# Kernel optimization log

Hardware: AMD Instinct MI355X
Metric: run time of the kernel (lower is better)

## Reference

```python
import jax, jax.numpy as jnp
import numpy as np

B, S, D = 2, 2048, 1024
H, DH = 16, 64
FF = 4 * D
EPS = 1e-5
SCALE = 1.0 / np.sqrt(DH)


def setup_inputs() -> dict:
    key = jax.random.key(0)
    ks = jax.random.split(key, 8)
    std = 0.02
    return {
        "x": jax.random.normal(ks[0], (B, S, D), jnp.float32),
        "ln1_g": jnp.ones((D,), jnp.float32),
        "ln1_b": jnp.zeros((D,), jnp.float32),
        "w_qkv": jax.random.normal(ks[1], (D, 3 * H * DH), jnp.float32) * std,
        "b_qkv": jnp.zeros((3 * H * DH,), jnp.float32),
        "w_ao": jax.random.normal(ks[2], (H * DH, D), jnp.float32) * std,
        "b_ao": jnp.zeros((D,), jnp.float32),
        "ln2_g": jnp.ones((D,), jnp.float32),
        "ln2_b": jnp.zeros((D,), jnp.float32),
        "w_fc": jax.random.normal(ks[3], (D, FF), jnp.float32) * std,
        "b_fc": jnp.zeros((FF,), jnp.float32),
        "w_proj": jax.random.normal(ks[4], (FF, D), jnp.float32) * std,
        "b_proj": jnp.zeros((D,), jnp.float32),
    }


def _layernorm(x, g, b):
    mu = jnp.mean(x, axis=-1, keepdims=True)
    var = jnp.mean(jnp.square(x - mu), axis=-1, keepdims=True)
    return (x - mu) * jax.lax.rsqrt(var + EPS) * g + b


def reference(x, ln1_g, ln1_b, w_qkv, b_qkv, w_ao, b_ao,
              ln2_g, ln2_b, w_fc, b_fc, w_proj, b_proj):
    # pre-LN attention
    h = _layernorm(x, ln1_g, ln1_b)
    qkv = h @ w_qkv + b_qkv                      # [B,S,3*H*DH]
    q, k, v = jnp.split(qkv, 3, axis=-1)
    def heads(t):                                 # [B,S,H*DH] -> [B,H,S,DH]
        return t.reshape(B, S, H, DH).transpose(0, 2, 1, 3)
    q, k, v = heads(q), heads(k), heads(v)
    scores = jnp.einsum("bhsd,bhtd->bhst", q, k) * SCALE  # full [B,H,S,S]
    probs = jax.nn.softmax(scores, axis=-1)
    attn = jnp.einsum("bhst,bhtd->bhsd", probs, v)        # [B,H,S,DH]
    attn = attn.transpose(0, 2, 1, 3).reshape(B, S, H * DH)
    attn = attn @ w_ao + b_ao
    x = x + attn
    # pre-LN MLP (exact erf GELU, matches nn.GELU())
    h = _layernorm(x, ln2_g, ln2_b)
    h = jax.nn.gelu(h @ w_fc + b_fc, approximate=False)
    h = h @ w_proj + b_proj
    return x + h
```

## Files before the change

### kernel.cpp

```cpp
#include <hip/hip_runtime.h>
#include <hip/hip_bf16.h>

using short8 = __attribute__((ext_vector_type(8))) short;
using f32x4  = __attribute__((ext_vector_type(4))) float;

#define DEV __device__ __forceinline__

DEV unsigned short f2b(float f) {
  union { float f; unsigned u; } cv; cv.f = f;
  unsigned r = (cv.u + 0x7fffu + ((cv.u >> 16) & 1u)) >> 16;
  return (unsigned short)r;
}

typedef const __attribute__((address_space(1))) unsigned int* gp1;
typedef __attribute__((address_space(3))) unsigned int* lp3;
DEV void gl16(const void* g, void* l) {
  __builtin_amdgcn_global_load_lds((gp1)g, (lp3)l, 16, 0, 0);
}

__global__ void k_tcvt(const float* __restrict__ src, unsigned short* __restrict__ dst,
                       int K, int N) {
  __shared__ float tile[32][33];
  int n0 = blockIdx.x * 32, k0 = blockIdx.y * 32;
  int tx = threadIdx.x, ty = threadIdx.y;
#pragma unroll
  for (int j = 0; j < 4; ++j)
    tile[ty + j * 8][tx] = src[(size_t)(k0 + ty + j * 8) * N + (n0 + tx)];
  __syncthreads();
#pragma unroll
  for (int j = 0; j < 4; ++j)
    dst[(size_t)(n0 + ty + j * 8) * K + (k0 + tx)] = f2b(tile[tx][ty + j * 8]);
}

__global__ void k_tv(const unsigned short* __restrict__ src, unsigned short* __restrict__ dst) {
  __shared__ unsigned short tile[32][33];
  int d0 = blockIdx.x * 32, s0 = blockIdx.y * 32;
  size_t base = (size_t)blockIdx.z * 2048 * 64;
  int tx = threadIdx.x, ty = threadIdx.y;
#pragma unroll
  for (int j = 0; j < 4; ++j)
    tile[ty + j * 8][tx] = src[base + (size_t)(s0 + ty + j * 8) * 64 + (d0 + tx)];
  __syncthreads();
#pragma unroll
  for (int j = 0; j < 4; ++j)
    dst[base + (size_t)(d0 + ty + j * 8) * 2048 + (s0 + tx)] = tile[tx][ty + j * 8];
}

__global__ __launch_bounds__(256) void k_ln(const float* __restrict__ x,
                                            const float* __restrict__ g,
                                            const float* __restrict__ b,
                                            unsigned short* __restrict__ y) {
  int row = blockIdx.x, tid = threadIdx.x;
  float4 v = reinterpret_cast<const float4*>(x + (size_t)row * 1024)[tid];
  float s  = v.x + v.y + v.z + v.w;
  float s2 = v.x * v.x + v.y * v.y + v.z * v.z + v.w * v.w;
#pragma unroll
  for (int m = 1; m < 64; m <<= 1) { s += __shfl_xor(s, m); s2 += __shfl_xor(s2, m); }
  __shared__ float ps[8];
  int w = tid >> 6;
  if ((tid & 63) == 0) { ps[w] = s; ps[4 + w] = s2; }
  __syncthreads();
  s  = ps[0] + ps[1] + ps[2] + ps[3];
  s2 = ps[4] + ps[5] + ps[6] + ps[7];
  float mu   = s * (1.0f / 1024.0f);
  float var  = fmaxf(s2 * (1.0f / 1024.0f) - mu * mu, 0.f);
  float rstd = rsqrtf(var + 1e-5f);
  float4 gv = reinterpret_cast<const float4*>(g)[tid];
  float4 bv = reinterpret_cast<const float4*>(b)[tid];
  ushort4 o;
  o.x = f2b((v.x - mu) * rstd * gv.x + bv.x);
  o.y = f2b((v.y - mu) * rstd * gv.y + bv.y);
  o.z = f2b((v.z - mu) * rstd * gv.z + bv.z);
  o.w = f2b((v.w - mu) * rstd * gv.w + bv.w);
  reinterpret_cast<ushort4*>(y + (size_t)row * 1024)[tid] = o;
}

enum { EPI_QKV = 0, EPI_RESID = 1, EPI_GELU = 2 };

template <int EPI>
__global__ __launch_bounds__(512, 2) void k_gemm256(
    const unsigned short* __restrict__ A, const unsigned short* __restrict__ BT,
    const float* __restrict__ bias, int M, int N, int K,
    unsigned short* __restrict__ outb,
    unsigned short* __restrict__ qb, unsigned short* __restrict__ kb,
    unsigned short* __restrict__ vb) {
  __shared__ __align__(16) unsigned short Abuf[2][256][64];
  __shared__ __align__(16) unsigned short Bbuf[2][256][64];
  int nx = gridDim.x, nwg = nx * gridDim.y;
  int w0 = blockIdx.y * nx + blockIdx.x;
  int id = (w0 & 7) * (nwg >> 3) + (w0 >> 3);
  int bx = id % nx, by = id / nx;
  int m0 = by * 256, n0 = bx * 256;
  int tid = threadIdx.x;
  int lane = tid & 63, wid = tid >> 6;
  int wm = wid >> 2, wn = wid & 3;
  int l15 = lane & 15, g = lane >> 4;
  int swl = l15 & 7;
  int lrow = lane >> 3;
  int lchunk = (lane & 7) ^ lrow;
  const unsigned short* Asrc = A  + (size_t)(m0 + wid * 32 + lrow) * K + lchunk * 8;
  const unsigned short* Bsrc = BT + (size_t)(n0 + wid * 32 + lrow) * K + lchunk * 8;
  auto stage = [&](int buf, int k0) {
#pragma unroll
    for (int i = 0; i < 4; ++i)
      gl16(Asrc + k0 + (size_t)i * 8 * K, &Abuf[buf][wid * 32 + i * 8][0]);
#pragma unroll
    for (int i = 0; i < 4; ++i)
      gl16(Bsrc + k0 + (size_t)i * 8 * K, &Bbuf[buf][wid * 32 + i * 8][0]);
  };
  f32x4 acc[8][4] = {};
  int nt = K >> 6;
  stage(0, 0);
  stage(1, 64);
  asm volatile("s_waitcnt vmcnt(8)" ::: "memory");
  __builtin_amdgcn_sched_barrier(0);
  __builtin_amdgcn_s_barrier();
  int cur = 0;
  for (int t = 0; t < nt; ++t) {
    const unsigned short (*As)[64] = Abuf[cur];
    const unsigned short (*Bs)[64] = Bbuf[cur];
    short8 a0[8], b0[4], a1[8], b1[4];
#pragma unroll
    for (int mi = 0; mi < 8; ++mi)
      a0[mi] = *reinterpret_cast<const short8*>(&As[wm * 128 + mi * 16 + l15][(g ^ swl) * 8]);
#pragma unroll
    for (int ni = 0; ni < 4; ++ni)
      b0[ni] = *reinterpret_cast<const short8*>(&Bs[wn * 64 + ni * 16 + l15][(g ^ swl) * 8]);
    __builtin_amdgcn_s_setprio(1);
#pragma unroll
    for (int mi = 0; mi < 8; ++mi)
#pragma unroll
      for (int ni = 0; ni < 4; ++ni)
        acc[mi][ni] = __builtin_amdgcn_mfma_f32_16x16x32_bf16(a0[mi], b0[ni], acc[mi][ni], 0, 0, 0);
    __builtin_amdgcn_s_setprio(0);
#pragma unroll
    for (int mi = 0; mi < 8; ++mi)
      a1[mi] = *reinterpret_cast<const short8*>(&As[wm * 128 + mi * 16 + l15][((4 + g) ^ swl) * 8]);
#pragma unroll
    for (int ni = 0; ni < 4; ++ni)
      b1[ni] = *reinterpret_cast<const short8*>(&Bs[wn * 64 + ni * 16 + l15][((4 + g) ^ swl) * 8]);
    asm volatile("s_waitcnt lgkmcnt(0)" ::: "memory");
    __builtin_amdgcn_sched_barrier(0);
    __builtin_amdgcn_s_barrier();
    __builtin_amdgcn_sched_barrier(0);
    if (t + 2 < nt) stage(cur, (t + 2) << 6);
    __builtin_amdgcn_s_setprio(1);
#pragma unroll
    for (int mi = 0; mi < 8; ++mi)
#pragma unroll
      for (int ni = 0; ni < 4; ++ni)
        acc[mi][ni] = __builtin_amdgcn_mfma_f32_16x16x32_bf16(a1[mi], b1[ni], acc[mi][ni], 0, 0, 0);
    __builtin_amdgcn_s_setprio(0);
    if (t + 2 < nt) {
      asm volatile("s_waitcnt vmcnt(8)" ::: "memory");
    } else if (t + 1 < nt) {
      asm volatile("s_waitcnt vmcnt(0)" ::: "memory");
    }
    __builtin_amdgcn_sched_barrier(0);
    __builtin_amdgcn_s_barrier();
    cur ^= 1;
  }
#pragma unroll
  for (int mi = 0; mi < 8; ++mi) {
#pragma unroll
    for (int ni = 0; ni < 4; ++ni) {
      int row0 = m0 + wm * 128 + mi * 16 + g * 4;
      int col  = n0 + wn * 64 + ni * 16 + l15;
      float bcol = bias[col];
#pragma unroll
      for (int j = 0; j < 4; ++j) {
        int r = row0 + j;
        float vv = acc[mi][ni][j] + bcol;
        if (EPI == EPI_QKV) {
          int which = col >> 10;
          int hc = col & 1023;
          int h = hc >> 6, d = hc & 63;
          int bb = r >> 11, ss = r & 2047;
          size_t idx = (((size_t)(bb * 16 + h)) * 2048 + ss) * 64 + d;
          unsigned short bv_ = f2b(which == 0 ? vv * 0.18033688011112042f : vv);
          if (which == 0)      qb[idx] = bv_;
          else if (which == 1) kb[idx] = bv_;
          else                 vb[idx] = bv_;
        } else {
          float ge = 0.5f * vv * (1.0f + erff(vv * 0.70710678118654752f));
          outb[(size_t)r * N + col] = f2b(ge);
        }
      }
    }
  }
}

__global__ __launch_bounds__(512) void k_gemm512(
    const unsigned short* __restrict__ A, const unsigned short* __restrict__ BT,
    const float* __restrict__ bias, int M, int N, int K,
    float* __restrict__ outf, const float* __restrict__ resid) {
  __shared__ __align__(16) unsigned short Abuf[2][128][64];
  __shared__ __align__(16) unsigned short Bbuf[2][128][64];
  int nx = gridDim.x, nwg = nx * gridDim.y;
  int w0 = blockIdx.y * nx + blockIdx.x;
  int id = (w0 & 7) * (nwg >> 3) + (w0 >> 3);
  int bx = id % nx, by = id / nx;
  int m0 = by * 128, n0 = bx * 128;
  int tid = threadIdx.x;
  int lane = tid & 63, wid = tid >> 6;
  int wm = wid >> 2, wn = wid & 3;
  int l15 = lane & 15, g = lane >> 4;
  int swl = l15 & 7;
  int lrow = lane >> 3;
  int lchunk = (lane & 7) ^ lrow;
  const unsigned short* Asrc = A  + (size_t)(m0 + wid * 16 + lrow) * K + lchunk * 8;
  const unsigned short* Bsrc = BT + (size_t)(n0 + wid * 16 + lrow) * K + lchunk * 8;
  auto stage = [&](int buf, int k0) {
#pragma unroll
    for (int i = 0; i < 2; ++i)
      gl16(Asrc + k0 + (size_t)i * 8 * K, &Abuf[buf][wid * 16 + i * 8][0]);
#pragma unroll
    for (int i = 0; i < 2; ++i)
      gl16(Bsrc + k0 + (size_t)i * 8 * K, &Bbuf[buf][wid * 16 + i * 8][0]);
  };
  f32x4 acc[4][2] = {};
  int nt = K >> 6;
  stage(0, 0);
  stage(1, 64);
  asm volatile("s_waitcnt vmcnt(4)" ::: "memory");
  __builtin_amdgcn_sched_barrier(0);
  __builtin_amdgcn_s_barrier();
  int cur = 0;
  for (int t = 0; t < nt; ++t) {
    const unsigned short (*As)[64] = Abuf[cur];
    const unsigned short (*Bs)[64] = Bbuf[cur];
    short8 a0[4], b0[2], a1[4], b1[2];
#pragma unroll
    for (int mi = 0; mi < 4; ++mi)
      a0[mi] = *reinterpret_cast<const short8*>(&As[wm * 64 + mi * 16 + l15][(g ^ swl) * 8]);
#pragma unroll
    for (int ni = 0; ni < 2; ++ni)
      b0[ni] = *reinterpret_cast<const short8*>(&Bs[wn * 32 + ni * 16 + l15][(g ^ swl) * 8]);
    __builtin_amdgcn_s_setprio(1);
#pragma unroll
    for (int mi = 0; mi < 4; ++mi)
#pragma unroll
      for (int ni = 0; ni < 2; ++ni)
        acc[mi][ni] = __builtin_amdgcn_mfma_f32_16x16x32_bf16(a0[mi], b0[ni], acc[mi][ni], 0, 0, 0);
    __builtin_amdgcn_s_setprio(0);
#pragma unroll
    for (int mi = 0; mi < 4; ++mi)
      a1[mi] = *reinterpret_cast<const short8*>(&As[wm * 64 + mi * 16 + l15][((4 + g) ^ swl) * 8]);
#pragma unroll
    for (int ni = 0; ni < 2; ++ni)
      b1[ni] = *reinterpret_cast<const short8*>(&Bs[wn * 32 + ni * 16 + l15][((4 + g) ^ swl) * 8]);
    asm volatile("s_waitcnt lgkmcnt(0)" ::: "memory");
    __builtin_amdgcn_sched_barrier(0);
    __builtin_amdgcn_s_barrier();
    __builtin_amdgcn_sched_barrier(0);
    if (t + 2 < nt) stage(cur, (t + 2) << 6);
    __builtin_amdgcn_s_setprio(1);
#pragma unroll
    for (int mi = 0; mi < 4; ++mi)
#pragma unroll
      for (int ni = 0; ni < 2; ++ni)
        acc[mi][ni] = __builtin_amdgcn_mfma_f32_16x16x32_bf16(a1[mi], b1[ni], acc[mi][ni], 0, 0, 0);
    __builtin_amdgcn_s_setprio(0);
    if (t + 2 < nt) {
      asm volatile("s_waitcnt vmcnt(4)" ::: "memory");
    } else if (t + 1 < nt) {
      asm volatile("s_waitcnt vmcnt(0)" ::: "memory");
    }
    __builtin_amdgcn_sched_barrier(0);
    __builtin_amdgcn_s_barrier();
    cur ^= 1;
  }
#pragma unroll
  for (int mi = 0; mi < 4; ++mi) {
#pragma unroll
    for (int ni = 0; ni < 2; ++ni) {
      int row0 = m0 + wm * 64 + mi * 16 + g * 4;
      int col  = n0 + wn * 32 + ni * 16 + l15;
      float bcol = bias[col];
#pragma unroll
      for (int j = 0; j < 4; ++j) {
        size_t idx = (size_t)(row0 + j) * N + col;
        outf[idx] = acc[mi][ni][j] + bcol + resid[idx];
      }
    }
  }
}

__global__ __launch_bounds__(256) void k_attn(
    const unsigned short* __restrict__ qb, const unsigned short* __restrict__ kb,
    const unsigned short* __restrict__ vt, unsigned short* __restrict__ attn_out) {
  __shared__ __align__(16) unsigned short Ks[64][64];
  __shared__ __align__(16) unsigned short Vs[64][64];
  __shared__ __align__(16) unsigned short Plds[4][16][72];
  int bh = blockIdx.y;
  int b = bh >> 4, h = bh & 15;
  int tid = threadIdx.x;
  int lane = tid & 63, wid = tid >> 6;
  int l15 = lane & 15, g = lane >> 4;
  int q0 = blockIdx.x * 64 + wid * 16;
  const unsigned short* Qb = qb + (size_t)bh * 2048 * 64;
  const unsigned short* Kb = kb + (size_t)bh * 2048 * 64;
  const unsigned short* Vt = vt + (size_t)bh * 64 * 2048;
  short8 qf0 = *reinterpret_cast<const short8*>(&Qb[(size_t)(q0 + l15) * 64 + g * 8]);
  short8 qf1 = *reinterpret_cast<const short8*>(&Qb[(size_t)(q0 + l15) * 64 + 32 + g * 8]);
  float mj = -1e30f, lj = 0.f;
  f32x4 o[4] = {};
  int sr  = wid * 16 + (lane >> 3);
  int scn = (lane & 7) ^ (sr & 7);
  int swl = l15 & 7;
  for (int t0 = 0; t0 < 2048; t0 += 64) {
    __syncthreads();
    gl16(Kb + (size_t)(t0 + sr) * 64 + scn * 8,       &Ks[wid * 16][0]);
    gl16(Kb + (size_t)(t0 + sr + 8) * 64 + scn * 8,   &Ks[wid * 16 + 8][0]);
    gl16(Vt + (size_t)sr * 2048 + t0 + scn * 8,       &Vs[wid * 16][0]);
    gl16(Vt + (size_t)(sr + 8) * 2048 + t0 + scn * 8, &Vs[wid * 16 + 8][0]);
    __syncthreads();
    f32x4 scv[4];
#pragma unroll
    for (int kk = 0; kk < 4; ++kk) {
      short8 kf0 = *reinterpret_cast<const short8*>(&Ks[kk * 16 + l15][(g ^ swl) * 8]);
      short8 kf1 = *reinterpret_cast<const short8*>(&Ks[kk * 16 + l15][((4 + g) ^ swl) * 8]);
      f32x4 z = {};
      z = __builtin_amdgcn_mfma_f32_16x16x32_bf16(kf0, qf0, z, 0, 0, 0);
      scv[kk] = __builtin_amdgcn_mfma_f32_16x16x32_bf16(kf1, qf1, z, 0, 0, 0);
    }
    float mx = -1e30f;
#pragma unroll
    for (int kk = 0; kk < 4; ++kk)
#pragma unroll
      for (int j = 0; j < 4; ++j) mx = fmaxf(mx, scv[kk][j]);
    mx = fmaxf(mx, __shfl_xor(mx, 16));
    mx = fmaxf(mx, __shfl_xor(mx, 32));
    bool skip = __all(mx <= mj + 8.0f);
    float mnew = skip ? mj : fmaxf(mj, mx);
    float p[16];
    float ts = 0.f;
#pragma unroll
    for (int kk = 0; kk < 4; ++kk)
#pragma unroll
      for (int j = 0; j < 4; ++j) {
        float pv = __builtin_amdgcn_exp2f(scv[kk][j] - mnew);
        p[kk * 4 + j] = pv;
        ts += pv;
      }
    ts += __shfl_xor(ts, 16);
    ts += __shfl_xor(ts, 32);
    if (!skip) {
      float ef = __builtin_amdgcn_exp2f(mj - mnew);
      int sb = 20 * g;
      float e0 = __shfl(ef, sb + 0), e1 = __shfl(ef, sb + 1);
      float e2 = __shfl(ef, sb + 2), e3 = __shfl(ef, sb + 3);
#pragma unroll
      for (int ct = 0; ct < 4; ++ct) {
        o[ct][0] *= e0; o[ct][1] *= e1; o[ct][2] *= e2; o[ct][3] *= e3;
      }
      lj = lj * ef + ts;
      mj = mnew;
    } else {
      lj += ts;
    }
#pragma unroll
    for (int kk = 0; kk < 4; ++kk) {
      unsigned r0, r1;
      asm("v_cvt_pk_bf16_f32 %0, %1, %2" : "=v"(r0) : "v"(p[kk * 4 + 0]), "v"(p[kk * 4 + 1]));
      asm("v_cvt_pk_bf16_f32 %0, %1, %2" : "=v"(r1) : "v"(p[kk * 4 + 2]), "v"(p[kk * 4 + 3]));
      unsigned long long w = (unsigned long long)r0 | ((unsigned long long)r1 << 32);
      *reinterpret_cast<unsigned long long*>(&Plds[wid][l15][kk * 16 + g * 4]) = w;
    }
    short8 pf0 = *reinterpret_cast<const short8*>(&Plds[wid][l15][g * 8]);
    short8 pf1 = *reinterpret_cast<const short8*>(&Plds[wid][l15][32 + g * 8]);
#pragma unroll
    for (int ct = 0; ct < 4; ++ct) {
      short8 vf0 = *reinterpret_cast<const short8*>(&Vs[ct * 16 + l15][(g ^ swl) * 8]);
      short8 vf1 = *reinterpret_cast<const short8*>(&Vs[ct * 16 + l15][((4 + g) ^ swl) * 8]);
      o[ct] = __builtin_amdgcn_mfma_f32_16x16x32_bf16(pf0, vf0, o[ct], 0, 0, 0);
      o[ct] = __builtin_amdgcn_mfma_f32_16x16x32_bf16(pf1, vf1, o[ct], 0, 0, 0);
    }
  }
  float invq = 1.0f / lj;
  int sb = 20 * g;
  float i0 = __shfl(invq, sb + 0), i1 = __shfl(invq, sb + 1);
  float i2 = __shfl(invq, sb + 2), i3 = __shfl(invq, sb + 3);
  float iv[4] = {i0, i1, i2, i3};
#pragma unroll
  for (int j = 0; j < 4; ++j) {
    size_t t = (size_t)b * 2048 + (q0 + g * 4 + j);
#pragma unroll
    for (int ct = 0; ct < 4; ++ct)
      attn_out[t * 1024 + h * 64 + ct * 16 + l15] = f2b(o[ct][j] * iv[j]);
  }
}

extern "C" void kernel_launch(void* const* d_in, const int* in_sizes, int n_in,
                              void* d_out, int out_size, void* d_ws, size_t ws_size,
                              hipStream_t stream) {
  (void)in_sizes; (void)n_in; (void)out_size; (void)ws_size;
  const float* x      = (const float*)d_in[0];
  const float* ln1_g  = (const float*)d_in[1];
  const float* ln1_b  = (const float*)d_in[2];
  const float* w_qkv  = (const float*)d_in[3];
  const float* b_qkv  = (const float*)d_in[4];
  const float* w_ao   = (const float*)d_in[5];
  const float* b_ao   = (const float*)d_in[6];
  const float* ln2_g  = (const float*)d_in[7];
  const float* ln2_b  = (const float*)d_in[8];
  const float* w_fc   = (const float*)d_in[9];
  const float* b_fc   = (const float*)d_in[10];
  const float* w_proj = (const float*)d_in[11];
  const float* b_proj = (const float*)d_in[12];
  float* out = (float*)d_out;

  char* ws = (char*)d_ws;
  size_t o = 0;
  auto nxt = [&](size_t bytes) { void* p = ws + o; o += (bytes + 255) & ~(size_t)255; return p; };
  unsigned short* wT_qkv  = (unsigned short*)nxt((size_t)3072 * 1024 * 2);
  unsigned short* wT_ao   = (unsigned short*)nxt((size_t)1024 * 1024 * 2);
  unsigned short* wT_fc   = (unsigned short*)nxt((size_t)4096 * 1024 * 2);
  unsigned short* wT_proj = (unsigned short*)nxt((size_t)1024 * 4096 * 2);
  unsigned short* h_ln    = (unsigned short*)nxt((size_t)4096 * 1024 * 2);
  unsigned short* qbuf    = (unsigned short*)nxt((size_t)4096 * 1024 * 2);
  unsigned short* kbuf    = (unsigned short*)nxt((size_t)4096 * 1024 * 2);
  unsigned short* vbuf    = (unsigned short*)nxt((size_t)4096 * 1024 * 2);
  unsigned short* vtb     = (unsigned short*)nxt((size_t)4096 * 1024 * 2);
  float*          out1    = (float*)nxt((size_t)4096 * 1024 * 4);
  unsigned short* fc_buf  = qbuf;
  unsigned short* attn_o  = vbuf;

  dim3 b32(32, 8, 1);
  k_tcvt<<<dim3(96, 32), b32, 0, stream>>>(w_qkv, wT_qkv, 1024, 3072);
  k_tcvt<<<dim3(32, 32), b32, 0, stream>>>(w_ao, wT_ao, 1024, 1024);
  k_tcvt<<<dim3(128, 32), b32, 0, stream>>>(w_fc, wT_fc, 1024, 4096);
  k_tcvt<<<dim3(32, 128), b32, 0, stream>>>(w_proj, wT_proj, 4096, 1024);

  k_ln<<<4096, 256, 0, stream>>>(x, ln1_g, ln1_b, h_ln);
  k_gemm256<EPI_QKV><<<dim3(12, 16), 512, 0, stream>>>(h_ln, wT_qkv, b_qkv, 4096, 3072, 1024,
                                                       nullptr, qbuf, kbuf, vbuf);
  k_tv<<<dim3(2, 64, 32), b32, 0, stream>>>(vbuf, vtb);
  k_attn<<<dim3(32, 32), 256, 0, stream>>>(qbuf, kbuf, vtb, attn_o);
  k_gemm512<<<dim3(8, 32), 512, 0, stream>>>(attn_o, wT_ao, b_ao, 4096, 1024, 1024,
                                             out1, x);
  k_ln<<<4096, 256, 0, stream>>>(out1, ln2_g, ln2_b, h_ln);
  k_gemm256<EPI_GELU><<<dim3(16, 16), 512, 0, stream>>>(h_ln, wT_fc, b_fc, 4096, 4096, 1024,
                                                        fc_buf, nullptr, nullptr, nullptr);
  k_gemm512<<<dim3(8, 32), 512, 0, stream>>>(fc_buf, wT_proj, b_proj, 4096, 1024, 4096,
                                             out, out1);
}
```

Before: 257.8 us.

## Double-buffer K/V tiles in attention and raise wave priority around MFMAs

The attention kernel now uses two LDS buffers for K and V and issues the async global-to-LDS loads for the next tile before computing on the current one, waiting only on the older loads via a vmcnt count. This is meant to overlap global memory latency with the QK and PV MFMA work instead of stalling on every tile. It also raises wave priority around the MFMA groups with s_setprio. In exchange it doubles K/V LDS use, which may lower occupancy, and it depends on exact vmcnt bookkeeping and manual barriers for correctness.

```diff
diff --git a/kernel.cpp b/kernel.cpp
--- a/kernel.cpp
+++ b/kernel.cpp
@@ -289,8 +289,8 @@
 __global__ __launch_bounds__(256) void k_attn(
     const unsigned short* __restrict__ qb, const unsigned short* __restrict__ kb,
     const unsigned short* __restrict__ vt, unsigned short* __restrict__ attn_out) {
-  __shared__ __align__(16) unsigned short Ks[64][64];
-  __shared__ __align__(16) unsigned short Vs[64][64];
+  __shared__ __align__(16) unsigned short Ks[2][64][64];
+  __shared__ __align__(16) unsigned short Vs[2][64][64];
   __shared__ __align__(16) unsigned short Plds[4][16][72];
   int bh = blockIdx.y;
   int b = bh >> 4, h = bh & 15;
@@ -308,21 +308,36 @@
   int sr  = wid * 16 + (lane >> 3);
   int scn = (lane & 7) ^ (sr & 7);
   int swl = l15 & 7;
+  auto stageKV = [&](int buf, int t0) {
+    gl16(Kb + (size_t)(t0 + sr) * 64 + scn * 8,       &Ks[buf][wid * 16][0]);
+    gl16(Kb + (size_t)(t0 + sr + 8) * 64 + scn * 8,   &Ks[buf][wid * 16 + 8][0]);
+    gl16(Vt + (size_t)sr * 2048 + t0 + scn * 8,       &Vs[buf][wid * 16][0]);
+    gl16(Vt + (size_t)(sr + 8) * 2048 + t0 + scn * 8, &Vs[buf][wid * 16 + 8][0]);
+  };
+  stageKV(0, 0);
+  int cur = 0;
   for (int t0 = 0; t0 < 2048; t0 += 64) {
-    __syncthreads();
-    gl16(Kb + (size_t)(t0 + sr) * 64 + scn * 8,       &Ks[wid * 16][0]);
-    gl16(Kb + (size_t)(t0 + sr + 8) * 64 + scn * 8,   &Ks[wid * 16 + 8][0]);
-    gl16(Vt + (size_t)sr * 2048 + t0 + scn * 8,       &Vs[wid * 16][0]);
-    gl16(Vt + (size_t)(sr + 8) * 2048 + t0 + scn * 8, &Vs[wid * 16 + 8][0]);
-    __syncthreads();
+    __builtin_amdgcn_s_barrier();
+    __builtin_amdgcn_sched_barrier(0);
+    if (t0 + 64 < 2048) {
+      stageKV(cur ^ 1, t0 + 64);
+      asm volatile("s_waitcnt vmcnt(4)" ::: "memory");
+    } else {
+      asm volatile("s_waitcnt vmcnt(0)" ::: "memory");
+    }
+    __builtin_amdgcn_sched_barrier(0);
+    __builtin_amdgcn_s_barrier();
+    __builtin_amdgcn_sched_barrier(0);
     f32x4 scv[4];
 #pragma unroll
     for (int kk = 0; kk < 4; ++kk) {
-      short8 kf0 = *reinterpret_cast<const short8*>(&Ks[kk * 16 + l15][(g ^ swl) * 8]);
-      short8 kf1 = *reinterpret_cast<const short8*>(&Ks[kk * 16 + l15][((4 + g) ^ swl) * 8]);
+      short8 kf0 = *reinterpret_cast<const short8*>(&Ks[cur][kk * 16 + l15][(g ^ swl) * 8]);
+      short8 kf1 = *reinterpret_cast<const short8*>(&Ks[cur][kk * 16 + l15][((4 + g) ^ swl) * 8]);
       f32x4 z = {};
+      __builtin_amdgcn_s_setprio(1);
       z = __builtin_amdgcn_mfma_f32_16x16x32_bf16(kf0, qf0, z, 0, 0, 0);
       scv[kk] = __builtin_amdgcn_mfma_f32_16x16x32_bf16(kf1, qf1, z, 0, 0, 0);
+      __builtin_amdgcn_s_setprio(0);
     }
     float mx = -1e30f;
 #pragma unroll
@@ -371,11 +386,14 @@
     short8 pf1 = *reinterpret_cast<const short8*>(&Plds[wid][l15][32 + g * 8]);
 #pragma unroll
     for (int ct = 0; ct < 4; ++ct) {
-      short8 vf0 = *reinterpret_cast<const short8*>(&Vs[ct * 16 + l15][(g ^ swl) * 8]);
-      short8 vf1 = *reinterpret_cast<const short8*>(&Vs[ct * 16 + l15][((4 + g) ^ swl) * 8]);
+      short8 vf0 = *reinterpret_cast<const short8*>(&Vs[cur][ct * 16 + l15][(g ^ swl) * 8]);
+      short8 vf1 = *reinterpret_cast<const short8*>(&Vs[cur][ct * 16 + l15][((4 + g) ^ swl) * 8]);
+      __builtin_amdgcn_s_setprio(1);
       o[ct] = __builtin_amdgcn_mfma_f32_16x16x32_bf16(pf0, vf0, o[ct], 0, 0, 0);
       o[ct] = __builtin_amdgcn_mfma_f32_16x16x32_bf16(pf1, vf1, o[ct], 0, 0, 0);
-    }
+      __builtin_amdgcn_s_setprio(0);
+    }
+    cur ^= 1;
   }
   float invq = 1.0f / lj;
   int sb = 20 * g;
```

Measured after the change: 282.3 us. 1.09x slower.

## Process two query tiles per wave in attention to reuse K/V tiles

Applied to the files above, without the earlier changes.

Each wave in the attention kernel now handles 32 query rows (two 16-row sub-tiles) instead of 16, so each block covers 128 queries and the grid is halved. Every K/V tile loaded into LDS is reused for twice as many queries, which halves global K/V traffic and the number of barrier rounds. The MFMA groups are also wrapped in s_setprio raises. In exchange the kernel uses more registers and launches only 512 blocks, which lowers occupancy and parallelism across the CUs.

```diff
diff --git a/kernel.cpp b/kernel.cpp
--- a/kernel.cpp
+++ b/kernel.cpp
@@ -291,20 +291,24 @@
     const unsigned short* __restrict__ vt, unsigned short* __restrict__ attn_out) {
   __shared__ __align__(16) unsigned short Ks[64][64];
   __shared__ __align__(16) unsigned short Vs[64][64];
-  __shared__ __align__(16) unsigned short Plds[4][16][72];
+  __shared__ __align__(16) unsigned short Plds[4][2][16][72];
   int bh = blockIdx.y;
   int b = bh >> 4, h = bh & 15;
   int tid = threadIdx.x;
   int lane = tid & 63, wid = tid >> 6;
   int l15 = lane & 15, g = lane >> 4;
-  int q0 = blockIdx.x * 64 + wid * 16;
+  int q0 = blockIdx.x * 128 + wid * 32;
   const unsigned short* Qb = qb + (size_t)bh * 2048 * 64;
   const unsigned short* Kb = kb + (size_t)bh * 2048 * 64;
   const unsigned short* Vt = vt + (size_t)bh * 64 * 2048;
-  short8 qf0 = *reinterpret_cast<const short8*>(&Qb[(size_t)(q0 + l15) * 64 + g * 8]);
-  short8 qf1 = *reinterpret_cast<const short8*>(&Qb[(size_t)(q0 + l15) * 64 + 32 + g * 8]);
-  float mj = -1e30f, lj = 0.f;
-  f32x4 o[4] = {};
+  short8 qf[2][2];
+#pragma unroll
+  for (int qi = 0; qi < 2; ++qi)
+#pragma unroll
+    for (int c = 0; c < 2; ++c)
+      qf[qi][c] = *reinterpret_cast<const short8*>(&Qb[(size_t)(q0 + qi * 16 + l15) * 64 + c * 32 + g * 8]);
+  float mj[2] = {-1e30f, -1e30f}, lj[2] = {0.f, 0.f};
+  f32x4 o[2][4] = {};
   int sr  = wid * 16 + (lane >> 3);
   int scn = (lane & 7) ^ (sr & 7);
   int swl = l15 & 7;
@@ -315,79 +319,99 @@
     gl16(Vt + (size_t)sr * 2048 + t0 + scn * 8,       &Vs[wid * 16][0]);
     gl16(Vt + (size_t)(sr + 8) * 2048 + t0 + scn * 8, &Vs[wid * 16 + 8][0]);
     __syncthreads();
-    f32x4 scv[4];
+    f32x4 scv[2][4];
 #pragma unroll
     for (int kk = 0; kk < 4; ++kk) {
       short8 kf0 = *reinterpret_cast<const short8*>(&Ks[kk * 16 + l15][(g ^ swl) * 8]);
       short8 kf1 = *reinterpret_cast<const short8*>(&Ks[kk * 16 + l15][((4 + g) ^ swl) * 8]);
-      f32x4 z = {};
-      z = __builtin_amdgcn_mfma_f32_16x16x32_bf16(kf0, qf0, z, 0, 0, 0);
-      scv[kk] = __builtin_amdgcn_mfma_f32_16x16x32_bf16(kf1, qf1, z, 0, 0, 0);
-    }
-    float mx = -1e30f;
-#pragma unroll
-    for (int kk = 0; kk < 4; ++kk)
-#pragma unroll
-      for (int j = 0; j < 4; ++j) mx = fmaxf(mx, scv[kk][j]);
-    mx = fmaxf(mx, __shfl_xor(mx, 16));
-    mx = fmaxf(mx, __shfl_xor(mx, 32));
-    bool skip = __all(mx <= mj + 8.0f);
-    float mnew = skip ? mj : fmaxf(mj, mx);
-    float p[16];
-    float ts = 0.f;
-#pragma unroll
-    for (int kk = 0; kk < 4; ++kk)
-#pragma unroll
-      for (int j = 0; j < 4; ++j) {
-        float pv = __builtin_amdgcn_exp2f(scv[kk][j] - mnew);
-        p[kk * 4 + j] = pv;
-        ts += pv;
-      }
-    ts += __shfl_xor(ts, 16);
-    ts += __shfl_xor(ts, 32);
-    if (!skip) {
-      float ef = __builtin_amdgcn_exp2f(mj - mnew);
-      int sb = 20 * g;
-      float e0 = __shfl(ef, sb + 0), e1 = __shfl(ef, sb + 1);
-      float e2 = __shfl(ef, sb + 2), e3 = __shfl(ef, sb + 3);
-#pragma unroll
-      for (int ct = 0; ct < 4; ++ct) {
-        o[ct][0] *= e0; o[ct][1] *= e1; o[ct][2] *= e2; o[ct][3] *= e3;
-      }
-      lj = lj * ef + ts;
-      mj = mnew;
-    } else {
-      lj += ts;
-    }
-#pragma unroll
-    for (int kk = 0; kk < 4; ++kk) {
-      unsigned r0, r1;
-      asm("v_cvt_pk_bf16_f32 %0, %1, %2" : "=v"(r0) : "v"(p[kk * 4 + 0]), "v"(p[kk * 4 + 1]));
-      asm("v_cvt_pk_bf16_f32 %0, %1, %2" : "=v"(r1) : "v"(p[kk * 4 + 2]), "v"(p[kk * 4 + 3]));
-      unsigned long long w = (unsigned long long)r0 | ((unsigned long long)r1 << 32);
-      *reinterpret_cast<unsigned long long*>(&Plds[wid][l15][kk * 16 + g * 4]) = w;
-    }
-    short8 pf0 = *reinterpret_cast<const short8*>(&Plds[wid][l15][g * 8]);
-    short8 pf1 = *reinterpret_cast<const short8*>(&Plds[wid][l15][32 + g * 8]);
+      __builtin_amdgcn_s_setprio(1);
+#pragma unroll
+      for (int qi = 0; qi < 2; ++qi) {
+        f32x4 z = {};
+        z = __builtin_amdgcn_mfma_f32_16x16x32_bf16(kf0, qf[qi][0], z, 0, 0, 0);
+        scv[qi][kk] = __builtin_amdgcn_mfma_f32_16x16x32_bf16(kf1, qf[qi][1], z, 0, 0, 0);
+      }
+      __builtin_amdgcn_s_setprio(0);
+    }
+    float p[2][16];
+#pragma unroll
+    for (int qi = 0; qi < 2; ++qi) {
+      float mx = -1e30f;
+#pragma unroll
+      for (int kk = 0; kk < 4; ++kk)
+#pragma unroll
+        for (int j = 0; j < 4; ++j) mx = fmaxf(mx, scv[qi][kk][j]);
+      mx = fmaxf(mx, __shfl_xor(mx, 16));
+      mx = fmaxf(mx, __shfl_xor(mx, 32));
+      bool skip = __all(mx <= mj[qi] + 8.0f);
+      float mnew = skip ? mj[qi] : fmaxf(mj[qi], mx);
+      float ts = 0.f;
+#pragma unroll
+      for (int kk = 0; kk < 4; ++kk)
+#pragma unroll
+        for (int j = 0; j < 4; ++j) {
+          float pv = __builtin_amdgcn_exp2f(scv[qi][kk][j] - mnew);
+          p[qi][kk * 4 + j] = pv;
+          ts += pv;
+        }
+      ts += __shfl_xor(ts, 16);
+      ts += __shfl_xor(ts, 32);
+      if (!skip) {
+        float ef = __builtin_amdgcn_exp2f(mj[qi] - mnew);
+        int sb = 20 * g;
+        float e0 = __shfl(ef, sb + 0), e1 = __shfl(ef, sb + 1);
+        float e2 = __shfl(ef, sb + 2), e3 = __shfl(ef, sb + 3);
+#pragma unroll
+        for (int ct = 0; ct < 4; ++ct) {
+          o[qi][ct][0] *= e0; o[qi][ct][1] *= e1; o[qi][ct][2] *= e2; o[qi][ct][3] *= e3;
+        }
+        lj[qi] = lj[qi] * ef + ts;
+        mj[qi] = mnew;
+      } else {
+        lj[qi] += ts;
+      }
+#pragma unroll
+      for (int kk = 0; kk < 4; ++kk) {
+        unsigned r0, r1;
+        asm("v_cvt_pk_bf16_f32 %0, %1, %2" : "=v"(r0) : "v"(p[qi][kk * 4 + 0]), "v"(p[qi][kk * 4 + 1]));
+        asm("v_cvt_pk_bf16_f32 %0, %1, %2" : "=v"(r1) : "v"(p[qi][kk * 4 + 2]), "v"(p[qi][kk * 4 + 3]));
+        unsigned long long w = (unsigned long long)r0 | ((unsigned long long)r1 << 32);
+        *reinterpret_cast<unsigned long long*>(&Plds[wid][qi][l15][kk * 16 + g * 4]) = w;
+      }
+    }
+    short8 pf[2][2];
+#pragma unroll
+    for (int qi = 0; qi < 2; ++qi) {
+      pf[qi][0] = *reinterpret_cast<const short8*>(&Plds[wid][qi][l15][g * 8]);
+      pf[qi][1] = *reinterpret_cast<const short8*>(&Plds[wid][qi][l15][32 + g * 8]);
+    }
 #pragma unroll
     for (int ct = 0; ct < 4; ++ct) {
       short8 vf0 = *reinterpret_cast<const short8*>(&Vs[ct * 16 + l15][(g ^ swl) * 8]);
       short8 vf1 = *reinterpret_cast<const short8*>(&Vs[ct * 16 + l15][((4 + g) ^ swl) * 8]);
-      o[ct] = __builtin_amdgcn_mfma_f32_16x16x32_bf16(pf0, vf0, o[ct], 0, 0, 0);
-      o[ct] = __builtin_amdgcn_mfma_f32_16x16x32_bf16(pf1, vf1, o[ct], 0, 0, 0);
-    }
-  }
-  float invq = 1.0f / lj;
-  int sb = 20 * g;
-  float i0 = __shfl(invq, sb + 0), i1 = __shfl(invq, sb + 1);
-  float i2 = __shfl(invq, sb + 2), i3 = __shfl(invq, sb + 3);
-  float iv[4] = {i0, i1, i2, i3};
-#pragma unroll
-  for (int j = 0; j < 4; ++j) {
-    size_t t = (size_t)b * 2048 + (q0 + g * 4 + j);
-#pragma unroll
-    for (int ct = 0; ct < 4; ++ct)
-      attn_out[t * 1024 + h * 64 + ct * 16 + l15] = f2b(o[ct][j] * iv[j]);
+      __builtin_amdgcn_s_setprio(1);
+#pragma unroll
+      for (int qi = 0; qi < 2; ++qi) {
+        o[qi][ct] = __builtin_amdgcn_mfma_f32_16x16x32_bf16(pf[qi][0], vf0, o[qi][ct], 0, 0, 0);
+        o[qi][ct] = __builtin_amdgcn_mfma_f32_16x16x32_bf16(pf[qi][1], vf1, o[qi][ct], 0, 0, 0);
+      }
+      __builtin_amdgcn_s_setprio(0);
+    }
+  }
+#pragma unroll
+  for (int qi = 0; qi < 2; ++qi) {
+    float invq = 1.0f / lj[qi];
+    int sb = 20 * g;
+    float i0 = __shfl(invq, sb + 0), i1 = __shfl(invq, sb + 1);
+    float i2 = __shfl(invq, sb + 2), i3 = __shfl(invq, sb + 3);
+    float iv[4] = {i0, i1, i2, i3};
+#pragma unroll
+    for (int j = 0; j < 4; ++j) {
+      size_t t = (size_t)b * 2048 + (q0 + qi * 16 + g * 4 + j);
+#pragma unroll
+      for (int ct = 0; ct < 4; ++ct)
+        attn_out[t * 1024 + h * 64 + ct * 16 + l15] = f2b(o[qi][ct][j] * iv[j]);
+    }
   }
 }
 
@@ -436,7 +460,7 @@
   k_gemm256<EPI_QKV><<<dim3(12, 16), 512, 0, stream>>>(h_ln, wT_qkv, b_qkv, 4096, 3072, 1024,
                                                        nullptr, qbuf, kbuf, vbuf);
   k_tv<<<dim3(2, 64, 32), b32, 0, stream>>>(vbuf, vtb);
-  k_attn<<<dim3(32, 32), 256, 0, stream>>>(qbuf, kbuf, vtb, attn_o);
+  k_attn<<<dim3(16, 32), 256, 0, stream>>>(qbuf, kbuf, vtb, attn_o);
   k_gemm512<<<dim3(8, 32), 512, 0, stream>>>(attn_o, wT_ao, b_ao, 4096, 1024, 1024,
                                              out1, x);
   k_ln<<<4096, 256, 0, stream>>>(out1, ln2_g, ln2_b, h_ln);
```

Measured after the change: 265.2 us. 1.03x slower.

## Restructure 256x256 GEMM main loop into four-quadrant ping-pong schedule

Applied to the files above, without the earlier changes.

The GEMM inner loop moves from a prefetch-distance-2 schedule with two K-halves to a one-ahead double buffer. Each K tile is split into four quadrant MFMA phases, with interleaved LDS fragment reads and staggered global-to-LDS loads (A first, then B), separated by workgroup barriers. The goal is a finer-grained interleaving of memory and matrix-core work, in the style of a ping-pong between waves. The cost is a shallower prefetch (vmcnt(0) every iteration), more barriers per tile, and the loss of K-dimension double-buffer lookahead.

```diff
diff --git a/kernel.cpp b/kernel.cpp
--- a/kernel.cpp
+++ b/kernel.cpp
@@ -96,66 +96,106 @@
   int wm = wid >> 2, wn = wid & 3;
   int l15 = lane & 15, g = lane >> 4;
   int swl = l15 & 7;
-  int lrow = lane >> 3;
-  int lchunk = (lane & 7) ^ lrow;
-  const unsigned short* Asrc = A  + (size_t)(m0 + wid * 32 + lrow) * K + lchunk * 8;
-  const unsigned short* Bsrc = BT + (size_t)(n0 + wid * 32 + lrow) * K + lchunk * 8;
-  auto stage = [&](int buf, int k0) {
-#pragma unroll
-    for (int i = 0; i < 4; ++i)
-      gl16(Asrc + k0 + (size_t)i * 8 * K, &Abuf[buf][wid * 32 + i * 8][0]);
-#pragma unroll
-    for (int i = 0; i < 4; ++i)
-      gl16(Bsrc + k0 + (size_t)i * 8 * K, &Bbuf[buf][wid * 32 + i * 8][0]);
+  int lrow8 = lane >> 3;
+  int lch   = (lane & 7) ^ lrow8;
+  auto stageA = [&](int buf, int t, int half) {
+#pragma unroll
+    for (int i = 0; i < 2; ++i) {
+      int rl = half * 128 + i * 64 + wid * 8;
+      gl16(A + (size_t)(m0 + rl + lrow8) * K + (t << 6) + lch * 8, &Abuf[buf][rl][0]);
+    }
+  };
+  auto stageB = [&](int buf, int t, int half) {
+#pragma unroll
+    for (int i = 0; i < 2; ++i) {
+      int rl = half * 128 + i * 64 + wid * 8;
+      gl16(BT + (size_t)(n0 + rl + lrow8) * K + (t << 6) + lch * 8, &Bbuf[buf][rl][0]);
+    }
   };
   f32x4 acc[8][4] = {};
   int nt = K >> 6;
-  stage(0, 0);
-  stage(1, 64);
-  asm volatile("s_waitcnt vmcnt(8)" ::: "memory");
+  stageA(0, 0, 0); stageA(0, 0, 1);
+  stageB(0, 0, 0); stageB(0, 0, 1);
+  asm volatile("s_waitcnt vmcnt(0)" ::: "memory");
   __builtin_amdgcn_sched_barrier(0);
   __builtin_amdgcn_s_barrier();
   int cur = 0;
   for (int t = 0; t < nt; ++t) {
     const unsigned short (*As)[64] = Abuf[cur];
     const unsigned short (*Bs)[64] = Bbuf[cur];
-    short8 a0[8], b0[4], a1[8], b1[4];
-#pragma unroll
-    for (int mi = 0; mi < 8; ++mi)
-      a0[mi] = *reinterpret_cast<const short8*>(&As[wm * 128 + mi * 16 + l15][(g ^ swl) * 8]);
-#pragma unroll
-    for (int ni = 0; ni < 4; ++ni)
-      b0[ni] = *reinterpret_cast<const short8*>(&Bs[wn * 64 + ni * 16 + l15][(g ^ swl) * 8]);
-    __builtin_amdgcn_s_setprio(1);
-#pragma unroll
-    for (int mi = 0; mi < 8; ++mi)
-#pragma unroll
-      for (int ni = 0; ni < 4; ++ni)
-        acc[mi][ni] = __builtin_amdgcn_mfma_f32_16x16x32_bf16(a0[mi], b0[ni], acc[mi][ni], 0, 0, 0);
-    __builtin_amdgcn_s_setprio(0);
-#pragma unroll
-    for (int mi = 0; mi < 8; ++mi)
-      a1[mi] = *reinterpret_cast<const short8*>(&As[wm * 128 + mi * 16 + l15][((4 + g) ^ swl) * 8]);
-#pragma unroll
-    for (int ni = 0; ni < 4; ++ni)
-      b1[ni] = *reinterpret_cast<const short8*>(&Bs[wn * 64 + ni * 16 + l15][((4 + g) ^ swl) * 8]);
+    int nb = cur ^ 1;
+    short8 afr[4][2], bfr[2][2][2];
+#pragma unroll
+    for (int mi = 0; mi < 4; ++mi) {
+      afr[mi][0] = *reinterpret_cast<const short8*>(&As[wm * 128 + mi * 16 + l15][(g ^ swl) * 8]);
+      afr[mi][1] = *reinterpret_cast<const short8*>(&As[wm * 128 + mi * 16 + l15][((4 + g) ^ swl) * 8]);
+    }
+#pragma unroll
+    for (int ni = 0; ni < 2; ++ni) {
+      bfr[0][ni][0] = *reinterpret_cast<const short8*>(&Bs[wn * 64 + ni * 16 + l15][(g ^ swl) * 8]);
+      bfr[0][ni][1] = *reinterpret_cast<const short8*>(&Bs[wn * 64 + ni * 16 + l15][((4 + g) ^ swl) * 8]);
+    }
+    if (t + 1 < nt) { stageA(nb, t + 1, 0); stageA(nb, t + 1, 1); }
+    __builtin_amdgcn_s_barrier();
     asm volatile("s_waitcnt lgkmcnt(0)" ::: "memory");
     __builtin_amdgcn_sched_barrier(0);
-    __builtin_amdgcn_s_barrier();
-    __builtin_amdgcn_sched_barrier(0);
-    if (t + 2 < nt) stage(cur, (t + 2) << 6);
-    __builtin_amdgcn_s_setprio(1);
-#pragma unroll
-    for (int mi = 0; mi < 8; ++mi)
-#pragma unroll
-      for (int ni = 0; ni < 4; ++ni)
-        acc[mi][ni] = __builtin_amdgcn_mfma_f32_16x16x32_bf16(a1[mi], b1[ni], acc[mi][ni], 0, 0, 0);
-    __builtin_amdgcn_s_setprio(0);
-    if (t + 2 < nt) {
-      asm volatile("s_waitcnt vmcnt(8)" ::: "memory");
-    } else if (t + 1 < nt) {
-      asm volatile("s_waitcnt vmcnt(0)" ::: "memory");
-    }
+    __builtin_amdgcn_s_setprio(1);
+#pragma unroll
+    for (int mi = 0; mi < 4; ++mi)
+#pragma unroll
+      for (int ni = 0; ni < 2; ++ni) {
+        acc[mi][ni] = __builtin_amdgcn_mfma_f32_16x16x32_bf16(afr[mi][0], bfr[0][ni][0], acc[mi][ni], 0, 0, 0);
+        acc[mi][ni] = __builtin_amdgcn_mfma_f32_16x16x32_bf16(afr[mi][1], bfr[0][ni][1], acc[mi][ni], 0, 0, 0);
+      }
+    __builtin_amdgcn_s_setprio(0);
+    __builtin_amdgcn_s_barrier();
+#pragma unroll
+    for (int ni = 0; ni < 2; ++ni) {
+      bfr[1][ni][0] = *reinterpret_cast<const short8*>(&Bs[wn * 64 + (2 + ni) * 16 + l15][(g ^ swl) * 8]);
+      bfr[1][ni][1] = *reinterpret_cast<const short8*>(&Bs[wn * 64 + (2 + ni) * 16 + l15][((4 + g) ^ swl) * 8]);
+    }
+    if (t + 1 < nt) { stageB(nb, t + 1, 0); stageB(nb, t + 1, 1); }
+    __builtin_amdgcn_s_barrier();
+    asm volatile("s_waitcnt lgkmcnt(0)" ::: "memory");
+    __builtin_amdgcn_sched_barrier(0);
+    __builtin_amdgcn_s_setprio(1);
+#pragma unroll
+    for (int mi = 0; mi < 4; ++mi)
+#pragma unroll
+      for (int ni = 0; ni < 2; ++ni) {
+        acc[mi][2 + ni] = __builtin_amdgcn_mfma_f32_16x16x32_bf16(afr[mi][0], bfr[1][ni][0], acc[mi][2 + ni], 0, 0, 0);
+        acc[mi][2 + ni] = __builtin_amdgcn_mfma_f32_16x16x32_bf16(afr[mi][1], bfr[1][ni][1], acc[mi][2 + ni], 0, 0, 0);
+      }
+    __builtin_amdgcn_s_setprio(0);
+    __builtin_amdgcn_s_barrier();
+#pragma unroll
+    for (int mi = 0; mi < 4; ++mi) {
+      afr[mi][0] = *reinterpret_cast<const short8*>(&As[wm * 128 + (4 + mi) * 16 + l15][(g ^ swl) * 8]);
+      afr[mi][1] = *reinterpret_cast<const short8*>(&As[wm * 128 + (4 + mi) * 16 + l15][((4 + g) ^ swl) * 8]);
+    }
+    __builtin_amdgcn_s_barrier();
+    asm volatile("s_waitcnt lgkmcnt(0)" ::: "memory");
+    __builtin_amdgcn_sched_barrier(0);
+    __builtin_amdgcn_s_setprio(1);
+#pragma unroll
+    for (int mi = 0; mi < 4; ++mi)
+#pragma unroll
+      for (int ni = 0; ni < 2; ++ni) {
+        acc[4 + mi][2 + ni] = __builtin_amdgcn_mfma_f32_16x16x32_bf16(afr[mi][0], bfr[1][ni][0], acc[4 + mi][2 + ni], 0, 0, 0);
+        acc[4 + mi][2 + ni] = __builtin_amdgcn_mfma_f32_16x16x32_bf16(afr[mi][1], bfr[1][ni][1], acc[4 + mi][2 + ni], 0, 0, 0);
+      }
+    __builtin_amdgcn_s_setprio(0);
+    __builtin_amdgcn_s_barrier();
+    __builtin_amdgcn_s_setprio(1);
+#pragma unroll
+    for (int mi = 0; mi < 4; ++mi)
+#pragma unroll
+      for (int ni = 0; ni < 2; ++ni) {
+        acc[4 + mi][ni] = __builtin_amdgcn_mfma_f32_16x16x32_bf16(afr[mi][0], bfr[0][ni][0], acc[4 + mi][ni], 0, 0, 0);
+        acc[4 + mi][ni] = __builtin_amdgcn_mfma_f32_16x16x32_bf16(afr[mi][1], bfr[0][ni][1], acc[4 + mi][ni], 0, 0, 0);
+      }
+    __builtin_amdgcn_s_setprio(0);
+    asm volatile("s_waitcnt vmcnt(0)" ::: "memory");
     __builtin_amdgcn_sched_barrier(0);
     __builtin_amdgcn_s_barrier();
     cur ^= 1;
```

Result: no change. 262.7 us (+1.9%).
